# Performance work log

Measured on AMD Instinct MI355X. Metric: run time of the kernel, lower is better.

## Reference

```python
import jax, jax.numpy as jnp
import numpy as np

HIDDEN = 1024
NUM_HEADS = 16
HEAD_DIM = HIDDEN // NUM_HEADS


def setup_inputs() -> dict:
    key = jax.random.key(0)
    k1, k2, k3 = jax.random.split(key, 3)
    x = jax.random.normal(k1, (2, 2048, HIDDEN), dtype=jnp.float32)
    # Linear weights, torch layout [out_features, in_features]
    w_qkv = jax.random.normal(k2, (3 * HIDDEN, HIDDEN), dtype=jnp.float32) * 0.02
    w_out = jax.random.normal(k3, (HIDDEN, HIDDEN), dtype=jnp.float32) * 0.02
    return {"x": x, "w_qkv": w_qkv, "w_out": w_out}


def reference(x, w_qkv, w_out):
    B, S, H = x.shape
    scale = 1.0 / HEAD_DIM ** 0.5
    qkv = jnp.einsum('bsh,oh->bso', x, w_qkv)              # [B,S,3H]
    qkv = qkv.reshape(B, S, 3, NUM_HEADS, HEAD_DIM)
    qkv = jnp.transpose(qkv, (2, 0, 3, 1, 4))               # [3,B,nh,S,hd]
    q, k, v = qkv[0], qkv[1], qkv[2]
    scores = jnp.einsum('bnsd,bntd->bnst', q, k) * scale    # [B,nh,S,S]
    attn = jax.nn.softmax(scores, axis=-1)
    out = jnp.einsum('bnst,bntd->bnsd', attn, v)            # [B,nh,S,hd]
    out = jnp.transpose(out, (0, 2, 1, 3)).reshape(B, S, H)
    return jnp.einsum('bsh,oh->bso', out, w_out)
```

## Files before the change

kernel.cpp:

```cpp
#include <hip/hip_runtime.h>
#include <stdint.h>

typedef unsigned short u16;
typedef __bf16 bf16x8 __attribute__((ext_vector_type(8)));
typedef float f32x4 __attribute__((ext_vector_type(4)));
typedef float f32x16 __attribute__((ext_vector_type(16)));
typedef unsigned u32x4 __attribute__((ext_vector_type(4)));

#define DEVI __device__ __forceinline__

typedef __attribute__((address_space(1))) void gvoid;
typedef __attribute__((address_space(3))) void lvoid;

DEVI u16 f2b(float f) {
  unsigned x = __builtin_bit_cast(unsigned, f);
  return (u16)((x + 0x7fffu + ((x >> 16) & 1u)) >> 16);
}

DEVI float exp2g(float x) { return __builtin_amdgcn_exp2f(x); }

DEVI void gload_lds16(const void* g, void* l) {
  __builtin_amdgcn_global_load_lds((gvoid*)g, (lvoid*)l, 16, 0, 0);
}

#define QSCALE 0.18033688011112042f

__global__ void cast_x(const float* __restrict__ in, u16* __restrict__ out, int n4) {
  int i = blockIdx.x * 256 + threadIdx.x;
  int stride = gridDim.x * 256;
  for (; i < n4; i += stride) {
    float4 v = ((const float4*)in)[i];
    ushort4 o;
    o.x = f2b(v.x); o.y = f2b(v.y); o.z = f2b(v.z); o.w = f2b(v.w);
    ((ushort4*)out)[i] = o;
  }
}

__global__ void cast_w(const float* __restrict__ wqkv, const float* __restrict__ wout,
                       u16* __restrict__ outb) {
  int i = blockIdx.x * 256 + threadIdx.x;
  int stride = gridDim.x * 256;
  for (; i < 1048576; i += stride) {
    const float* src = (i < 786432) ? wqkv + 4 * (long)i : wout + 4 * (long)(i - 786432);
    float4 v = *(const float4*)src;
    if (i < 262144) { v.x *= QSCALE; v.y *= QSCALE; v.z *= QSCALE; v.w *= QSCALE; }
    ushort4 o;
    o.x = f2b(v.x); o.y = f2b(v.y); o.z = f2b(v.z); o.w = f2b(v.w);
    ((ushort4*)outb)[i] = o;
  }
}

template<int OUT>
__global__ __launch_bounds__(256)
void gemm_bt(const u16* __restrict__ A, const u16* __restrict__ B, void* __restrict__ Cv,
             void* __restrict__ Cv2, int M, int N, int K) {
  __shared__ u16 lA[128 * 64];
  __shared__ u16 lB[128 * 64];
  const int tid = threadIdx.x;
  const int lane = tid & 63;
  const int lr = lane & 15;
  const int lg = lane >> 4;
  const int wid = tid >> 6;
  const long bm = (long)blockIdx.y * 128;
  const long bn = (long)blockIdx.x * 128;
  const int wr = (wid >> 1) * 64;
  const int wc = (wid & 1) * 64;

  f32x4 acc[4][4];
#pragma unroll
  for (int i = 0; i < 4; ++i)
#pragma unroll
    for (int j = 0; j < 4; ++j)
      acc[i][j] = (f32x4){0.f, 0.f, 0.f, 0.f};

  for (int k0 = 0; k0 < K; k0 += 64) {
#pragma unroll
    for (int q = 0; q < 4; ++q) {
      int bi = tid + q * 256;
      int row = bi >> 3;
      int col = ((bi & 7) ^ (row & 7)) * 8;
      gload_lds16(A + (bm + row) * (long)K + k0 + col, (char*)lA + bi * 16);
    }
#pragma unroll
    for (int q = 0; q < 4; ++q) {
      int bi = tid + q * 256;
      int row = bi >> 3;
      int col = ((bi & 7) ^ (row & 7)) * 8;
      gload_lds16(B + (bn + row) * (long)K + k0 + col, (char*)lB + bi * 16);
    }
    __syncthreads();
#pragma unroll
    for (int kk = 0; kk < 2; ++kk) {
      bf16x8 af[4], bfr[4];
      int kb = kk * 4 + lg;
#pragma unroll
      for (int mi = 0; mi < 4; ++mi) {
        int row = wr + mi * 16 + lr;
        af[mi] = *(const bf16x8*)((const char*)lA + row * 128 + ((kb ^ (row & 7)) << 4));
      }
#pragma unroll
      for (int ni = 0; ni < 4; ++ni) {
        int row = wc + ni * 16 + lr;
        bfr[ni] = *(const bf16x8*)((const char*)lB + row * 128 + ((kb ^ (row & 7)) << 4));
      }
#pragma unroll
      for (int mi = 0; mi < 4; ++mi)
#pragma unroll
        for (int ni = 0; ni < 4; ++ni)
          acc[mi][ni] = __builtin_amdgcn_mfma_f32_16x16x32_bf16(af[mi], bfr[ni], acc[mi][ni], 0, 0, 0);
    }
    __syncthreads();
  }

  if (OUT == 2 && bn >= 2048) {
#pragma unroll
    for (int mi = 0; mi < 4; ++mi)
#pragma unroll
      for (int ni = 0; ni < 4; ++ni) {
        long tok = bm + wr + mi * 16 + lg * 4;
        long f = bn + wc + ni * 16 + lr - 2048;
        ushort4 st;
        st.x = f2b(acc[mi][ni][0]);
        st.y = f2b(acc[mi][ni][1]);
        st.z = f2b(acc[mi][ni][2]);
        st.w = f2b(acc[mi][ni][3]);
        u16* dst = (u16*)Cv2 + (((tok >> 11) << 4) + (f >> 6)) * 131072 + (f & 63) * 2048 + (tok & 2047);
        *(ushort4*)dst = st;
      }
  } else {
    const long strideN = (OUT == 2) ? 2048 : N;
#pragma unroll
    for (int mi = 0; mi < 4; ++mi)
#pragma unroll
      for (int ni = 0; ni < 4; ++ni)
#pragma unroll
        for (int r = 0; r < 4; ++r) {
          long row = bm + wr + mi * 16 + lg * 4 + r;
          long col = bn + wc + ni * 16 + lr;
          float v = acc[mi][ni][r];
          if (OUT == 1) ((float*)Cv)[row * strideN + col] = v;
          else          ((u16*)Cv)[row * strideN + col] = f2b(v);
        }
  }
}

__global__ __launch_bounds__(512, 4)
void attn_fwd(const u16* __restrict__ qk, const u16* __restrict__ vT,
              u16* __restrict__ outb) {
  __shared__ char SM[65536];

  const int tid = threadIdx.x;
  const int lane = tid & 63;
  const int wid = tid >> 6;
  const int ql = lane & 31;
  const int h  = lane >> 5;
  const int th = wid >> 2;
  const int qb = wid & 3;

  const int flat = blockIdx.x + (blockIdx.y << 4) + (blockIdx.z << 8);
  const int swz  = ((flat & 7) << 6) + (flat >> 3);
  const int qt = swz & 15;
  const int hd = (swz >> 4) & 15;
  const int b  = swz >> 8;

  const long rowbase = (long)b * 2048;
  const int qcol = hd * 64;
  const int kcol = 1024 + hd * 64;
  const int TSK = 64 * 2048;
  const long vhb = ((long)b * 16 + hd) * 131072;

  const int q0w = qt * 128 + qb * 32;
  bf16x8 qf[4];
  {
    const u16* qp = qk + (rowbase + q0w + ql) * 2048 + qcol + h * 8;
#pragma unroll
    for (int dblk = 0; dblk < 4; ++dblk)
      qf[dblk] = *(const bf16x8*)(qp + dblk * 16);
  }

  float l_r = 0.f;
  f32x16 o[2];
#pragma unroll
  for (int d = 0; d < 2; ++d)
#pragma unroll
    for (int r = 0; r < 16; ++r) o[d][r] = 0.f;

  const int rk = tid >> 3;
  const int ck = ((tid & 7) ^ (rk & 7)) * 8;
  const int dstb = tid * 16;
  const u16* kp = qk + (rowbase + rk) * 2048 + kcol + ck;
  const u16* vp = vT + vhb + rk * 2048 + ck;

  gload_lds16(kp, SM + dstb);                 gload_lds16(vp, SM + 32768 + dstb);
  gload_lds16(kp + TSK, SM + 8192 + dstb);    gload_lds16(vp + 64, SM + 40960 + dstb);
  kp += 2 * TSK; vp += 128;
  asm volatile("s_waitcnt vmcnt(2)" ::: "memory");
  __builtin_amdgcn_s_barrier();
  __builtin_amdgcn_sched_barrier(0);

  for (int tt = 0; tt < 8; ++tt) {
#pragma unroll
    for (int I = 0; I < 4; ++I) {
      char* KsCur = SM + I * 8192;
      char* KsNxt = SM + ((I + 2) & 3) * 8192;
      char* VsCur = SM + 32768 + I * 8192;
      char* VsNxt = SM + 32768 + ((I + 2) & 3) * 8192;

      gload_lds16(kp, KsNxt + dstb);  kp += TSK;
      gload_lds16(vp, VsNxt + dstb);  vp += 64;

      f32x16 s;
#pragma unroll
      for (int r = 0; r < 16; ++r) s[r] = 0.f;
      const char* Kb = KsCur + (th * 32 + ql) * 128;
      __builtin_amdgcn_s_setprio(1);
#pragma unroll
      for (int kd = 0; kd < 4; ++kd) {
        bf16x8 kf = *(const bf16x8*)(Kb + (((kd * 2 + h) ^ (ql & 7)) << 4));
        s = __builtin_amdgcn_mfma_f32_32x32x16_bf16(kf, qf[kd], s, 0, 0, 0);
      }
      __builtin_amdgcn_s_setprio(0);

#pragma unroll
      for (int r = 0; r < 16; ++r) s[r] = exp2g(s[r]);
      l_r += (((s[0] + s[1]) + (s[2] + s[3])) + ((s[4] + s[5]) + (s[6] + s[7])))
           + (((s[8] + s[9]) + (s[10] + s[11])) + ((s[12] + s[13]) + (s[14] + s[15])));

      unsigned w[8];
#pragma unroll
      for (int m = 0; m < 8; ++m)
        asm("v_cvt_pk_bf16_f32 %0, %1, %2" : "=v"(w[m]) : "v"(s[2 * m]), "v"(s[2 * m + 1]));

      bf16x8 pb[2];
#pragma unroll
      for (int ks = 0; ks < 2; ++ks) {
        unsigned a0 = w[4 * ks],     a2 = w[4 * ks + 2];
        unsigned a1 = w[4 * ks + 1], a3 = w[4 * ks + 3];
        asm("s_nop 1\n\tv_permlane32_swap_b32 %0, %1" : "+v"(a0), "+v"(a2));
        asm("s_nop 1\n\tv_permlane32_swap_b32 %0, %1" : "+v"(a1), "+v"(a3));
        u32x4 t; t[0] = a0; t[1] = a1; t[2] = a2; t[3] = a3;
        pb[ks] = __builtin_bit_cast(bf16x8, t);
      }

      __builtin_amdgcn_s_setprio(1);
#pragma unroll
      for (int dblk = 0; dblk < 2; ++dblk) {
        const char* Vb = VsCur + (dblk * 32 + ql) * 128;
#pragma unroll
        for (int ks = 0; ks < 2; ++ks) {
          bf16x8 vf = *(const bf16x8*)(Vb + (((th * 4 + ks * 2 + h) ^ (ql & 7)) << 4));
          o[dblk] = __builtin_amdgcn_mfma_f32_32x32x16_bf16(vf, pb[ks], o[dblk], 0, 0, 0);
        }
      }
      __builtin_amdgcn_s_setprio(0);

      asm volatile("s_waitcnt vmcnt(2)" ::: "memory");
      __builtin_amdgcn_s_barrier();
      __builtin_amdgcn_sched_barrier(0);
    }
  }

  asm volatile("s_waitcnt vmcnt(0)" ::: "memory");
  __syncthreads();

  float px = l_r, py = l_r;
  asm("s_nop 1\n\tv_permlane32_swap_b32 %0, %1" : "+v"(px), "+v"(py));
  float lw = l_r + (h ? px : py);

  if (th == 1) {
    char* reg = SM + qb * 8320;
#pragma unroll
    for (int dblk = 0; dblk < 2; ++dblk)
#pragma unroll
      for (int r = 0; r < 16; ++r) {
        int dl = dblk * 32 + (r & 3) + 8 * (r >> 2) + 4 * h;
        *(float*)(reg + dl * 128 + ql * 4) = o[dblk][r];
      }
    if (h == 0) *(float*)(reg + 8192 + ql * 4) = lw;
  }
  __syncthreads();
  if (th == 0) {
    const char* reg = SM + qb * 8320;
#pragma unroll
    for (int dblk = 0; dblk < 2; ++dblk)
#pragma unroll
      for (int r = 0; r < 16; ++r) {
        int dl = dblk * 32 + (r & 3) + 8 * (r >> 2) + 4 * h;
        o[dblk][r] += *(const float*)(reg + dl * 128 + ql * 4);
      }
    float inv = 1.0f / (lw + *(const float*)(reg + 8192 + ql * 4));
    long row = rowbase + q0w + ql;
#pragma unroll
    for (int dblk = 0; dblk < 2; ++dblk)
#pragma unroll
      for (int m = 0; m < 4; ++m) {
        ushort4 st;
        st.x = f2b(o[dblk][4 * m + 0] * inv);
        st.y = f2b(o[dblk][4 * m + 1] * inv);
        st.z = f2b(o[dblk][4 * m + 2] * inv);
        st.w = f2b(o[dblk][4 * m + 3] * inv);
        *(ushort4*)(outb + row * 1024 + qcol + dblk * 32 + 8 * m + 4 * h) = st;
      }
  }
}

extern "C" void kernel_launch(void* const* d_in, const int* in_sizes, int n_in,
                              void* d_out, int out_size, void* d_ws, size_t ws_size,
                              hipStream_t stream) {
  const float* x     = (const float*)d_in[0];
  const float* w_qkv = (const float*)d_in[1];
  const float* w_out = (const float*)d_in[2];
  float* out = (float*)d_out;

  char* ws = (char*)d_ws;
  u16* xb    = (u16*)(ws);
  u16* wqkvb = (u16*)(ws + 8388608);
  u16* woutb = (u16*)(ws + 14680064);
  u16* qk    = (u16*)(ws + 16777216);
  u16* vT    = (u16*)(ws + 33554432);
  u16* attn  = (u16*)(ws + 41943040);

  cast_x<<<1024, 256, 0, stream>>>(x, xb, 4096 * 1024 / 4);
  cast_w<<<1024, 256, 0, stream>>>(w_qkv, w_out, wqkvb);

  gemm_bt<2><<<dim3(24, 32), 256, 0, stream>>>(xb, wqkvb, qk, vT, 4096, 3072, 1024);

  attn_fwd<<<dim3(16, 16, 2), 512, 0, stream>>>(qk, vT, attn);

  gemm_bt<1><<<dim3(8, 32), 256, 0, stream>>>(attn, woutb, out, nullptr, 4096, 1024, 1024);
}
```

Baseline: 111.0 us.

## Double-buffer attention K/V in 128-key stages and use 64-row tiles for out-proj GEMM

The attention kernel's four-slot ring of 64-key K/V tiles is replaced by two 16KB halves that each hold 128 keys. Each stage computes two 64-key sub-blocks before one full vmcnt(0) wait and barrier, which halves the number of barriers but makes the prefetch depth coarser. The output-projection GEMM is templated to use 64-row M tiles, doubling its grid to 512 blocks to fill more CUs, at the cost of less B-tile reuse per block.

```diff
diff --git a/kernel.cpp b/kernel.cpp
--- a/kernel.cpp
+++ b/kernel.cpp
@@ -50,32 +50,33 @@
   }
 }
 
-template<int OUT>
+template<int OUT, int TM>
 __global__ __launch_bounds__(256)
 void gemm_bt(const u16* __restrict__ A, const u16* __restrict__ B, void* __restrict__ Cv,
              void* __restrict__ Cv2, int M, int N, int K) {
-  __shared__ u16 lA[128 * 64];
+  constexpr int MI = TM / 32;
+  __shared__ u16 lA[TM * 64];
   __shared__ u16 lB[128 * 64];
   const int tid = threadIdx.x;
   const int lane = tid & 63;
   const int lr = lane & 15;
   const int lg = lane >> 4;
   const int wid = tid >> 6;
-  const long bm = (long)blockIdx.y * 128;
+  const long bm = (long)blockIdx.y * TM;
   const long bn = (long)blockIdx.x * 128;
-  const int wr = (wid >> 1) * 64;
+  const int wr = (wid >> 1) * (TM / 2);
   const int wc = (wid & 1) * 64;
 
-  f32x4 acc[4][4];
-#pragma unroll
-  for (int i = 0; i < 4; ++i)
+  f32x4 acc[MI][4];
+#pragma unroll
+  for (int i = 0; i < MI; ++i)
 #pragma unroll
     for (int j = 0; j < 4; ++j)
       acc[i][j] = (f32x4){0.f, 0.f, 0.f, 0.f};
 
   for (int k0 = 0; k0 < K; k0 += 64) {
 #pragma unroll
-    for (int q = 0; q < 4; ++q) {
+    for (int q = 0; q < MI; ++q) {
       int bi = tid + q * 256;
       int row = bi >> 3;
       int col = ((bi & 7) ^ (row & 7)) * 8;
@@ -91,10 +92,10 @@
     __syncthreads();
 #pragma unroll
     for (int kk = 0; kk < 2; ++kk) {
-      bf16x8 af[4], bfr[4];
+      bf16x8 af[MI], bfr[4];
       int kb = kk * 4 + lg;
 #pragma unroll
-      for (int mi = 0; mi < 4; ++mi) {
+      for (int mi = 0; mi < MI; ++mi) {
         int row = wr + mi * 16 + lr;
         af[mi] = *(const bf16x8*)((const char*)lA + row * 128 + ((kb ^ (row & 7)) << 4));
       }
@@ -104,7 +105,7 @@
         bfr[ni] = *(const bf16x8*)((const char*)lB + row * 128 + ((kb ^ (row & 7)) << 4));
       }
 #pragma unroll
-      for (int mi = 0; mi < 4; ++mi)
+      for (int mi = 0; mi < MI; ++mi)
 #pragma unroll
         for (int ni = 0; ni < 4; ++ni)
           acc[mi][ni] = __builtin_amdgcn_mfma_f32_16x16x32_bf16(af[mi], bfr[ni], acc[mi][ni], 0, 0, 0);
@@ -114,7 +115,7 @@
 
   if (OUT == 2 && bn >= 2048) {
 #pragma unroll
-    for (int mi = 0; mi < 4; ++mi)
+    for (int mi = 0; mi < MI; ++mi)
 #pragma unroll
       for (int ni = 0; ni < 4; ++ni) {
         long tok = bm + wr + mi * 16 + lg * 4;
@@ -130,7 +131,7 @@
   } else {
     const long strideN = (OUT == 2) ? 2048 : N;
 #pragma unroll
-    for (int mi = 0; mi < 4; ++mi)
+    for (int mi = 0; mi < MI; ++mi)
 #pragma unroll
       for (int ni = 0; ni < 4; ++ni)
 #pragma unroll
@@ -166,7 +167,7 @@
   const long rowbase = (long)b * 2048;
   const int qcol = hd * 64;
   const int kcol = 1024 + hd * 64;
-  const int TSK = 64 * 2048;
+  const int TK = 128 * 2048;
   const long vhb = ((long)b * 16 + hd) * 131072;
 
   const int q0w = qt * 128 + qb * 32;
@@ -191,76 +192,82 @@
   const u16* kp = qk + (rowbase + rk) * 2048 + kcol + ck;
   const u16* vp = vT + vhb + rk * 2048 + ck;
 
-  gload_lds16(kp, SM + dstb);                 gload_lds16(vp, SM + 32768 + dstb);
-  gload_lds16(kp + TSK, SM + 8192 + dstb);    gload_lds16(vp + 64, SM + 40960 + dstb);
-  kp += 2 * TSK; vp += 128;
-  asm volatile("s_waitcnt vmcnt(2)" ::: "memory");
+  gload_lds16(kp,             SM + dstb);
+  gload_lds16(kp + 64 * 2048, SM + 8192 + dstb);
+  gload_lds16(vp,             SM + 32768 + dstb);
+  gload_lds16(vp + 64,        SM + 40960 + dstb);
+  kp += TK; vp += 128;
+  asm volatile("s_waitcnt vmcnt(0)" ::: "memory");
   __builtin_amdgcn_s_barrier();
   __builtin_amdgcn_sched_barrier(0);
 
   for (int tt = 0; tt < 8; ++tt) {
 #pragma unroll
-    for (int I = 0; I < 4; ++I) {
-      char* KsCur = SM + I * 8192;
-      char* KsNxt = SM + ((I + 2) & 3) * 8192;
-      char* VsCur = SM + 32768 + I * 8192;
-      char* VsNxt = SM + 32768 + ((I + 2) & 3) * 8192;
-
-      gload_lds16(kp, KsNxt + dstb);  kp += TSK;
-      gload_lds16(vp, VsNxt + dstb);  vp += 64;
-
-      f32x16 s;
-#pragma unroll
-      for (int r = 0; r < 16; ++r) s[r] = 0.f;
-      const char* Kb = KsCur + (th * 32 + ql) * 128;
-      __builtin_amdgcn_s_setprio(1);
-#pragma unroll
-      for (int kd = 0; kd < 4; ++kd) {
-        bf16x8 kf = *(const bf16x8*)(Kb + (((kd * 2 + h) ^ (ql & 7)) << 4));
-        s = __builtin_amdgcn_mfma_f32_32x32x16_bf16(kf, qf[kd], s, 0, 0, 0);
-      }
-      __builtin_amdgcn_s_setprio(0);
-
-#pragma unroll
-      for (int r = 0; r < 16; ++r) s[r] = exp2g(s[r]);
-      l_r += (((s[0] + s[1]) + (s[2] + s[3])) + ((s[4] + s[5]) + (s[6] + s[7])))
-           + (((s[8] + s[9]) + (s[10] + s[11])) + ((s[12] + s[13]) + (s[14] + s[15])));
-
-      unsigned w[8];
-#pragma unroll
-      for (int m = 0; m < 8; ++m)
-        asm("v_cvt_pk_bf16_f32 %0, %1, %2" : "=v"(w[m]) : "v"(s[2 * m]), "v"(s[2 * m + 1]));
-
-      bf16x8 pb[2];
-#pragma unroll
-      for (int ks = 0; ks < 2; ++ks) {
-        unsigned a0 = w[4 * ks],     a2 = w[4 * ks + 2];
-        unsigned a1 = w[4 * ks + 1], a3 = w[4 * ks + 3];
-        asm("s_nop 1\n\tv_permlane32_swap_b32 %0, %1" : "+v"(a0), "+v"(a2));
-        asm("s_nop 1\n\tv_permlane32_swap_b32 %0, %1" : "+v"(a1), "+v"(a3));
-        u32x4 t; t[0] = a0; t[1] = a1; t[2] = a2; t[3] = a3;
-        pb[ks] = __builtin_bit_cast(bf16x8, t);
-      }
-
-      __builtin_amdgcn_s_setprio(1);
-#pragma unroll
-      for (int dblk = 0; dblk < 2; ++dblk) {
-        const char* Vb = VsCur + (dblk * 32 + ql) * 128;
+    for (int P = 0; P < 2; ++P) {
+      char* KsCur = SM + P * 16384;
+      char* VsCur = SM + 32768 + P * 16384;
+      char* KsNxt = SM + (P ^ 1) * 16384;
+      char* VsNxt = SM + 32768 + (P ^ 1) * 16384;
+
+      gload_lds16(kp,             KsNxt + dstb);
+      gload_lds16(kp + 64 * 2048, KsNxt + 8192 + dstb);
+      gload_lds16(vp,             VsNxt + dstb);
+      gload_lds16(vp + 64,        VsNxt + 8192 + dstb);
+      kp += TK; vp += 128;
+
+#pragma unroll
+      for (int j = 0; j < 2; ++j) {
+        f32x16 s;
+#pragma unroll
+        for (int r = 0; r < 16; ++r) s[r] = 0.f;
+        const char* Kb = KsCur + j * 8192 + (th * 32 + ql) * 128;
+        __builtin_amdgcn_s_setprio(1);
+#pragma unroll
+        for (int kd = 0; kd < 4; ++kd) {
+          bf16x8 kf = *(const bf16x8*)(Kb + (((kd * 2 + h) ^ (ql & 7)) << 4));
+          s = __builtin_amdgcn_mfma_f32_32x32x16_bf16(kf, qf[kd], s, 0, 0, 0);
+        }
+        __builtin_amdgcn_s_setprio(0);
+
+#pragma unroll
+        for (int r = 0; r < 16; ++r) s[r] = exp2g(s[r]);
+        l_r += (((s[0] + s[1]) + (s[2] + s[3])) + ((s[4] + s[5]) + (s[6] + s[7])))
+             + (((s[8] + s[9]) + (s[10] + s[11])) + ((s[12] + s[13]) + (s[14] + s[15])));
+
+        unsigned w[8];
+#pragma unroll
+        for (int m = 0; m < 8; ++m)
+          asm("v_cvt_pk_bf16_f32 %0, %1, %2" : "=v"(w[m]) : "v"(s[2 * m]), "v"(s[2 * m + 1]));
+
+        bf16x8 pb[2];
 #pragma unroll
         for (int ks = 0; ks < 2; ++ks) {
-          bf16x8 vf = *(const bf16x8*)(Vb + (((th * 4 + ks * 2 + h) ^ (ql & 7)) << 4));
-          o[dblk] = __builtin_amdgcn_mfma_f32_32x32x16_bf16(vf, pb[ks], o[dblk], 0, 0, 0);
+          unsigned a0 = w[4 * ks],     a2 = w[4 * ks + 2];
+          unsigned a1 = w[4 * ks + 1], a3 = w[4 * ks + 3];
+          asm("s_nop 1\n\tv_permlane32_swap_b32 %0, %1" : "+v"(a0), "+v"(a2));
+          asm("s_nop 1\n\tv_permlane32_swap_b32 %0, %1" : "+v"(a1), "+v"(a3));
+          u32x4 t; t[0] = a0; t[1] = a1; t[2] = a2; t[3] = a3;
+          pb[ks] = __builtin_bit_cast(bf16x8, t);
         }
-      }
-      __builtin_amdgcn_s_setprio(0);
-
-      asm volatile("s_waitcnt vmcnt(2)" ::: "memory");
+
+        __builtin_amdgcn_s_setprio(1);
+#pragma unroll
+        for (int dblk = 0; dblk < 2; ++dblk) {
+          const char* Vb = VsCur + j * 8192 + (dblk * 32 + ql) * 128;
+#pragma unroll
+          for (int ks = 0; ks < 2; ++ks) {
+            bf16x8 vf = *(const bf16x8*)(Vb + (((th * 4 + ks * 2 + h) ^ (ql & 7)) << 4));
+            o[dblk] = __builtin_amdgcn_mfma_f32_32x32x16_bf16(vf, pb[ks], o[dblk], 0, 0, 0);
+          }
+        }
+        __builtin_amdgcn_s_setprio(0);
+      }
+
+      asm volatile("s_waitcnt vmcnt(0)" ::: "memory");
       __builtin_amdgcn_s_barrier();
       __builtin_amdgcn_sched_barrier(0);
     }
   }
-
-  asm volatile("s_waitcnt vmcnt(0)" ::: "memory");
   __syncthreads();
 
   float px = l_r, py = l_r;
@@ -323,9 +330,9 @@
   cast_x<<<1024, 256, 0, stream>>>(x, xb, 4096 * 1024 / 4);
   cast_w<<<1024, 256, 0, stream>>>(w_qkv, w_out, wqkvb);
 
-  gemm_bt<2><<<dim3(24, 32), 256, 0, stream>>>(xb, wqkvb, qk, vT, 4096, 3072, 1024);
+  gemm_bt<2, 128><<<dim3(24, 32), 256, 0, stream>>>(xb, wqkvb, qk, vT, 4096, 3072, 1024);
 
   attn_fwd<<<dim3(16, 16, 2), 512, 0, stream>>>(qk, vT, attn);
 
-  gemm_bt<1><<<dim3(8, 32), 256, 0, stream>>>(attn, woutb, out, nullptr, 4096, 1024, 1024);
-}
+  gemm_bt<1, 64><<<dim3(8, 64), 256, 0, stream>>>(attn, woutb, out, nullptr, 4096, 1024, 1024);
+}
```

Result: faster. 105.3 us (-5.1%).
